# Kernel tuning notes

Measured on AMD Instinct MI355X. Metric: run time of the kernel, lower is better.

Reference implementation:

```python
import jax, jax.numpy as jnp
import numpy as np


def _sobel_filters():
    # fil is the 3x3 smoothing kernel [[1,2,1],[2,4,2],[1,2,1]]
    fil = np.array([[1, 2, 1], [2, 4, 2], [1, 2, 1]], dtype=np.float32)
    fx = np.zeros((3, 3, 3), dtype=np.float32)
    fx[0, :, :] = fil
    fx[2, :, :] = -fil
    fy = np.zeros((3, 3, 3), dtype=np.float32)
    fy[:, 0, :] = fil
    fy[:, 2, :] = -fil
    fz = np.zeros((3, 3, 3), dtype=np.float32)
    fz[:, :, 0] = fil
    fz[:, :, 2] = -fil
    # Stack the three fixed (non-learned) filters as 3 output channels: [O=3, I=1, 3,3,3]
    return jnp.asarray(np.stack([fx, fy, fz])[:, None])


_FILT = _sobel_filters()
_DN = ('NCDHW', 'OIDHW', 'NCDHW')


def _grad3d(v):
    # v: [N,1,D,H,W] -> [N,3,D,H,W], padding=1 == SAME for 3x3x3 stride 1
    return jax.lax.conv_general_dilated(
        v, _FILT.astype(v.dtype), window_strides=(1, 1, 1),
        padding='SAME', dimension_numbers=_DN)


def setup_inputs() -> dict:
    key = jax.random.key(0)
    k1, k2 = jax.random.split(key)
    shape = (2, 1, 160, 192, 224)
    x = jax.random.normal(k1, shape, dtype=jnp.float32)
    y = jax.random.normal(k2, shape, dtype=jnp.float32)
    return {"x": x, "y": y}


def reference(x, y):
    gx = _grad3d(x)  # [N,3,D,H,W]
    gy = _grad3d(y)
    d2 = (gx - gy) ** 2
    # sum over the 3 directions of the per-direction MSE
    return jnp.sum(jnp.mean(d2, axis=(0, 2, 3, 4)))
```

## Files before the change

kernel.cpp:

```cpp
#include <hip/hip_runtime.h>


#define N_  2
#define D_  160
#define H_  192
#define W_  224

#define TW  64
#define TH  16
#define TD  8

constexpr int LROWS = TH + 2;
constexpr int LCW   = 18;
constexpr int LCOLS = LCW * 4;
constexpr float SCALE = 1.0f / ((float)N_ * D_ * H_ * W_);

__global__ __launch_bounds__(256, 6)
void grad_loss_kernel(const float* __restrict__ x, const float* __restrict__ y,
                      float* __restrict__ out) {
    __shared__ float plane[2][LROWS][LCOLS];
    __shared__ float wsum[4];

    const int tx  = threadIdx.x;
    const int ty  = threadIdx.y;
    const int tid = ty * 64 + tx;

    const int w0 = blockIdx.x * TW;
    const int h0 = blockIdx.y * TH;
    const int nchunks = D_ / TD;
    const int n  = blockIdx.z / nchunks;
    const int d0 = (blockIdx.z % nchunks) * TD;

    const size_t base = (size_t)n * D_ * H_ * W_;
    const bool active = (w0 + tx) < W_;

    float a0[4], a1[4], a2[4];
    float b0[4], b1[4], b2[4];
    float acc = 0.f;

    const int rbase = 4 * ty;

    for (int p = d0 - 1, it = 0; p <= d0 + TD; ++p, ++it) {
        float (*buf)[LCOLS] = plane[it & 1];
        const bool pin = (p >= 0) && (p < D_);
        for (int idx = tid; idx < LROWS * LCW; idx += 256) {
            int row = idx / LCW;
            int ci  = idx - row * LCW;
            int gh  = h0 - 1 + row;
            int gw0 = w0 - 4 + 4 * ci;
            float4 v = make_float4(0.f, 0.f, 0.f, 0.f);
            if (pin && (unsigned)gh < (unsigned)H_ && (unsigned)gw0 < (unsigned)W_) {
                size_t off = base + ((size_t)p * H_ + gh) * W_ + gw0;
                float4 a = *(const float4*)(x + off);
                float4 b = *(const float4*)(y + off);
                v = make_float4(a.x - b.x, a.y - b.y, a.z - b.z, a.w - b.w);
            }
            *(float4*)&buf[row][4 * ci] = v;
        }
        __syncthreads();

        float sw[6], gw_[6];
        #pragma unroll
        for (int r = 0; r < 6; ++r) {
            float a = buf[rbase + r][tx + 3];
            float b = buf[rbase + r][tx + 4];
            float c = buf[rbase + r][tx + 5];
            sw[r]  = a + 2.f * b + c;
            gw_[r] = a - c;
        }
        float n0[4], n1[4], n2[4];
        #pragma unroll
        for (int j = 0; j < 4; ++j) {
            n0[j] = sw[j] + 2.f * sw[j + 1] + sw[j + 2];
            n1[j] = sw[j] - sw[j + 2];
            n2[j] = gw_[j] + 2.f * gw_[j + 1] + gw_[j + 2];
        }

        if (it >= 2 && active) {
            #pragma unroll
            for (int j = 0; j < 4; ++j) {
                float gx = a0[j] - n0[j];
                float gy = a1[j] + 2.f * b1[j] + n1[j];
                float gz = a2[j] + 2.f * b2[j] + n2[j];
                acc = fmaf(gx, gx, acc);
                acc = fmaf(gy, gy, acc);
                acc = fmaf(gz, gz, acc);
            }
        }

        #pragma unroll
        for (int j = 0; j < 4; ++j) {
            a0[j] = b0[j]; a1[j] = b1[j]; a2[j] = b2[j];
            b0[j] = n0[j]; b1[j] = n1[j]; b2[j] = n2[j];
        }
    }

    #pragma unroll
    for (int off = 32; off > 0; off >>= 1)
        acc += __shfl_down(acc, off, 64);
    if (tx == 0) wsum[ty] = acc;
    __syncthreads();
    if (tid == 0) {
        float s = (wsum[0] + wsum[1]) + (wsum[2] + wsum[3]);
        atomicAdd(out, s * SCALE);
    }
}

extern "C" void kernel_launch(void* const* d_in, const int* in_sizes, int n_in,
                              void* d_out, int out_size, void* d_ws, size_t ws_size,
                              hipStream_t stream) {
    const float* x = (const float*)d_in[0];
    const float* y = (const float*)d_in[1];
    float* out = (float*)d_out;

    hipMemsetAsync(out, 0, sizeof(float), stream);

    dim3 block(TW, 256 / TW);
    dim3 grid((W_ + TW - 1) / TW,
              H_ / TH,
              N_ * (D_ / TD));
    grad_loss_kernel<<<grid, block, 0, stream>>>(x, y, out);
}
```

Before: 152.2 us.

## Prefetch next depth plane into registers and shrink tile height to single-pass staging

Tile height drops from 16 to 12, so the 14x18 float4 staging chunks fit one per thread. Each thread now precomputes its staging address once. The next depth plane of x and y is loaded into registers while the current plane is being computed, then written to the alternate shared buffer, leaving one barrier per iteration. This hides global-load latency behind the stencil arithmetic, at the cost of more halo rows per output row and extra live registers.

```diff
diff --git a/kernel.cpp b/kernel.cpp
--- a/kernel.cpp
+++ b/kernel.cpp
@@ -7,12 +7,14 @@
 #define W_  224
 
 #define TW  64
-#define TH  16
+#define TH  12
 #define TD  8
 
 constexpr int LROWS = TH + 2;
 constexpr int LCW   = 18;
 constexpr int LCOLS = LCW * 4;
+constexpr int NCHUNK = LROWS * LCW;
+constexpr int PS = H_ * W_;
 constexpr float SCALE = 1.0f / ((float)N_ * D_ * H_ * W_);
 
 __global__ __launch_bounds__(256, 6)
@@ -31,54 +33,63 @@
     const int n  = blockIdx.z / nchunks;
     const int d0 = (blockIdx.z % nchunks) * TD;
 
-    const size_t base = (size_t)n * D_ * H_ * W_;
+    const size_t base = (size_t)n * D_ * PS;
     const bool active = (w0 + tx) < W_;
 
-    float a0[4], a1[4], a2[4];
-    float b0[4], b1[4], b2[4];
+    const bool stager = tid < NCHUNK;
+    const int srow = tid / LCW;
+    const int sci  = tid - srow * LCW;
+    const int gh   = h0 - 1 + srow;
+    const int gw0  = w0 - 4 + 4 * sci;
+    const bool sok = stager && (unsigned)gh < (unsigned)H_ &&
+                     (unsigned)gw0 < (unsigned)W_;
+    const float* px = x + base + (size_t)gh * W_ + gw0;
+    const float* py = y + base + (size_t)gh * W_ + gw0;
+    float* const ldst0 = &plane[0][0][0] + (srow * LCOLS + 4 * sci);
+    float* const ldst1 = &plane[1][0][0] + (srow * LCOLS + 4 * sci);
+
+    float a0[3], a1[3], a2[3], b0[3], b1[3], b2[3];
     float acc = 0.f;
+    const int rbase = 3 * ty;
 
-    const int rbase = 4 * ty;
+    float4 rx = make_float4(0.f, 0.f, 0.f, 0.f), ry = rx;
+    if (sok && d0 - 1 >= 0) {
+        rx = *(const float4*)(px + (size_t)(d0 - 1) * PS);
+        ry = *(const float4*)(py + (size_t)(d0 - 1) * PS);
+    }
+    if (stager)
+        *(float4*)ldst0 = make_float4(rx.x - ry.x, rx.y - ry.y,
+                                      rx.z - ry.z, rx.w - ry.w);
+    rx = make_float4(0.f, 0.f, 0.f, 0.f); ry = rx;
+    if (sok) {
+        rx = *(const float4*)(px + (size_t)d0 * PS);
+        ry = *(const float4*)(py + (size_t)d0 * PS);
+    }
 
-    for (int p = d0 - 1, it = 0; p <= d0 + TD; ++p, ++it) {
+    for (int it = 0; it <= TD + 1; ++it) {
+        __syncthreads();
         float (*buf)[LCOLS] = plane[it & 1];
-        const bool pin = (p >= 0) && (p < D_);
-        for (int idx = tid; idx < LROWS * LCW; idx += 256) {
-            int row = idx / LCW;
-            int ci  = idx - row * LCW;
-            int gh  = h0 - 1 + row;
-            int gw0 = w0 - 4 + 4 * ci;
-            float4 v = make_float4(0.f, 0.f, 0.f, 0.f);
-            if (pin && (unsigned)gh < (unsigned)H_ && (unsigned)gw0 < (unsigned)W_) {
-                size_t off = base + ((size_t)p * H_ + gh) * W_ + gw0;
-                float4 a = *(const float4*)(x + off);
-                float4 b = *(const float4*)(y + off);
-                v = make_float4(a.x - b.x, a.y - b.y, a.z - b.z, a.w - b.w);
-            }
-            *(float4*)&buf[row][4 * ci] = v;
-        }
-        __syncthreads();
 
-        float sw[6], gw_[6];
+        float sw[5], gww[5];
         #pragma unroll
-        for (int r = 0; r < 6; ++r) {
+        for (int r = 0; r < 5; ++r) {
             float a = buf[rbase + r][tx + 3];
             float b = buf[rbase + r][tx + 4];
             float c = buf[rbase + r][tx + 5];
             sw[r]  = a + 2.f * b + c;
-            gw_[r] = a - c;
+            gww[r] = a - c;
         }
-        float n0[4], n1[4], n2[4];
+        float n0[3], n1[3], n2[3];
         #pragma unroll
-        for (int j = 0; j < 4; ++j) {
+        for (int j = 0; j < 3; ++j) {
             n0[j] = sw[j] + 2.f * sw[j + 1] + sw[j + 2];
             n1[j] = sw[j] - sw[j + 2];
-            n2[j] = gw_[j] + 2.f * gw_[j + 1] + gw_[j + 2];
+            n2[j] = gww[j] + 2.f * gww[j + 1] + gww[j + 2];
         }
 
         if (it >= 2 && active) {
             #pragma unroll
-            for (int j = 0; j < 4; ++j) {
+            for (int j = 0; j < 3; ++j) {
                 float gx = a0[j] - n0[j];
                 float gy = a1[j] + 2.f * b1[j] + n1[j];
                 float gz = a2[j] + 2.f * b2[j] + n2[j];
@@ -89,9 +100,26 @@
         }
 
         #pragma unroll
-        for (int j = 0; j < 4; ++j) {
+        for (int j = 0; j < 3; ++j) {
             a0[j] = b0[j]; a1[j] = b1[j]; a2[j] = b2[j];
             b0[j] = n0[j]; b1[j] = n1[j]; b2[j] = n2[j];
+        }
+
+        if (it < TD + 1) {
+            float4 nx = make_float4(0.f, 0.f, 0.f, 0.f), ny = nx;
+            if (it < TD) {
+                int q = d0 + it + 1;
+                if (sok && q < D_) {
+                    nx = *(const float4*)(px + (size_t)q * PS);
+                    ny = *(const float4*)(py + (size_t)q * PS);
+                }
+            }
+            if (stager) {
+                float* dst = (it & 1) ? ldst0 : ldst1;
+                *(float4*)dst = make_float4(rx.x - ry.x, rx.y - ry.y,
+                                            rx.z - ry.z, rx.w - ry.w);
+            }
+            rx = nx; ry = ny;
         }
     }
 
```

After: 152.0 us. About the same (-0.1%).

## Replace LDS plane staging with register loads and wavefront shuffles for W stencil

Applied to the files above, without the earlier changes.

Drops the shared-memory double-buffered plane and the per-plane __syncthreads. Each lane now loads its own column of six rows directly into registers and gets its W neighbours through __shfl_up/__shfl_down, with one-plane-ahead register prefetch in a fully unrolled depth loop. Each 64-lane wave produces 62 output columns, so the grid grows in W and edge columns are loaded redundantly. In exchange the loads become scalar instead of float4, and the extra halo lanes add redundant load work.

```diff
diff --git a/kernel.cpp b/kernel.cpp
--- a/kernel.cpp
+++ b/kernel.cpp
@@ -5,75 +5,86 @@
 #define D_  160
 #define H_  192
 #define W_  224
+#define PS  (H_ * W_)
 
-#define TW  64
-#define TH  16
-#define TD  8
+#define TD   8
+#define WOUT 62
 
-constexpr int LROWS = TH + 2;
-constexpr int LCW   = 18;
-constexpr int LCOLS = LCW * 4;
 constexpr float SCALE = 1.0f / ((float)N_ * D_ * H_ * W_);
 
 __global__ __launch_bounds__(256, 6)
 void grad_loss_kernel(const float* __restrict__ x, const float* __restrict__ y,
                       float* __restrict__ out) {
-    __shared__ float plane[2][LROWS][LCOLS];
     __shared__ float wsum[4];
 
-    const int tx  = threadIdx.x;
-    const int ty  = threadIdx.y;
-    const int tid = ty * 64 + tx;
+    const int tid  = threadIdx.x;
+    const int lane = tid & 63;
+    const int wv   = tid >> 6;
 
-    const int w0 = blockIdx.x * TW;
-    const int h0 = blockIdx.y * TH;
+    const int w  = blockIdx.x * WOUT + lane - 1;
+    const int h0 = blockIdx.y * 16 + wv * 4;
     const int nchunks = D_ / TD;
-    const int n  = blockIdx.z / nchunks;
+    const int nb = blockIdx.z / nchunks;
     const int d0 = (blockIdx.z % nchunks) * TD;
 
-    const size_t base = (size_t)n * D_ * H_ * W_;
-    const bool active = (w0 + tx) < W_;
+    const bool wok    = (unsigned)w < (unsigned)W_;
+    const bool active = (lane >= 1) && (lane <= 62) && wok;
 
-    float a0[4], a1[4], a2[4];
-    float b0[4], b1[4], b2[4];
+    bool hv[6];
+    #pragma unroll
+    for (int r = 0; r < 6; ++r)
+        hv[r] = (unsigned)(h0 - 1 + r) < (unsigned)H_;
+
+    const float* bx = x + (size_t)nb * D_ * PS;
+    const float* by = y + (size_t)nb * D_ * PS;
+    const int obase = h0 * W_ + w;
+
+    float a0[4], a1[4], a2[4], b0[4], b1[4], b2[4];
+    float vc[6];
     float acc = 0.f;
 
-    const int rbase = 4 * ty;
-
-    for (int p = d0 - 1, it = 0; p <= d0 + TD; ++p, ++it) {
-        float (*buf)[LCOLS] = plane[it & 1];
-        const bool pin = (p >= 0) && (p < D_);
-        for (int idx = tid; idx < LROWS * LCW; idx += 256) {
-            int row = idx / LCW;
-            int ci  = idx - row * LCW;
-            int gh  = h0 - 1 + row;
-            int gw0 = w0 - 4 + 4 * ci;
-            float4 v = make_float4(0.f, 0.f, 0.f, 0.f);
-            if (pin && (unsigned)gh < (unsigned)H_ && (unsigned)gw0 < (unsigned)W_) {
-                size_t off = base + ((size_t)p * H_ + gh) * W_ + gw0;
-                float4 a = *(const float4*)(x + off);
-                float4 b = *(const float4*)(y + off);
-                v = make_float4(a.x - b.x, a.y - b.y, a.z - b.z, a.w - b.w);
-            }
-            *(float4*)&buf[row][4 * ci] = v;
-        }
-        __syncthreads();
-
-        float sw[6], gw_[6];
+    {
+        const int p = d0 - 1;
+        const bool pin = p >= 0;
         #pragma unroll
         for (int r = 0; r < 6; ++r) {
-            float a = buf[rbase + r][tx + 3];
-            float b = buf[rbase + r][tx + 4];
-            float c = buf[rbase + r][tx + 5];
-            sw[r]  = a + 2.f * b + c;
-            gw_[r] = a - c;
+            float xv = 0.f, yv = 0.f;
+            if (pin && hv[r] && wok) {
+                int o = obase + p * PS + (r - 1) * W_;
+                xv = bx[o]; yv = by[o];
+            }
+            vc[r] = xv - yv;
+        }
+    }
+
+    #pragma unroll
+    for (int it = 0; it <= TD + 1; ++it) {
+        float xn[6], yn[6];
+        const int p = d0 + it;
+        const bool pref = (it <= TD) && (p < D_);
+        #pragma unroll
+        for (int r = 0; r < 6; ++r) {
+            xn[r] = 0.f; yn[r] = 0.f;
+            if (pref && hv[r] && wok) {
+                int o = obase + p * PS + (r - 1) * W_;
+                xn[r] = bx[o]; yn[r] = by[o];
+            }
+        }
+
+        float sw[6], gw[6];
+        #pragma unroll
+        for (int r = 0; r < 6; ++r) {
+            float L  = __shfl_up(vc[r], 1, 64);
+            float Rt = __shfl_down(vc[r], 1, 64);
+            sw[r] = (L + Rt) + 2.f * vc[r];
+            gw[r] = L - Rt;
         }
         float n0[4], n1[4], n2[4];
         #pragma unroll
         for (int j = 0; j < 4; ++j) {
             n0[j] = sw[j] + 2.f * sw[j + 1] + sw[j + 2];
             n1[j] = sw[j] - sw[j + 2];
-            n2[j] = gw_[j] + 2.f * gw_[j + 1] + gw_[j + 2];
+            n2[j] = gw[j] + 2.f * gw[j + 1] + gw[j + 2];
         }
 
         if (it >= 2 && active) {
@@ -93,12 +104,15 @@
             a0[j] = b0[j]; a1[j] = b1[j]; a2[j] = b2[j];
             b0[j] = n0[j]; b1[j] = n1[j]; b2[j] = n2[j];
         }
+
+        #pragma unroll
+        for (int r = 0; r < 6; ++r) vc[r] = xn[r] - yn[r];
     }
 
     #pragma unroll
     for (int off = 32; off > 0; off >>= 1)
-        acc += __shfl_down(acc, off, 64);
-    if (tx == 0) wsum[ty] = acc;
+        acc += __shfl_xor(acc, off, 64);
+    if (lane == 0) wsum[wv] = acc;
     __syncthreads();
     if (tid == 0) {
         float s = (wsum[0] + wsum[1]) + (wsum[2] + wsum[3]);
@@ -115,9 +129,9 @@
 
     hipMemsetAsync(out, 0, sizeof(float), stream);
 
-    dim3 block(TW, 256 / TW);
-    dim3 grid((W_ + TW - 1) / TW,
-              H_ / TH,
+    dim3 block(256);
+    dim3 grid((W_ + WOUT - 1) / WOUT,
+              H_ / 16,
               N_ * (D_ / TD));
     grad_loss_kernel<<<grid, block, 0, stream>>>(x, y, out);
 }
```

After: 149.6 us. Within noise of the previous version (-1.7%).
